# Kernel optimization log

Hardware: AMD Instinct MI355X
Metric: run time of the kernel (lower is better)

## Reference

```python
import jax, jax.numpy as jnp
import numpy as np

B, D_MODEL, D_MEM, H, N_MEM = 128, 1024, 64, 16, 4096


def setup_inputs() -> dict:
    key = jax.random.key(0)
    ks = jax.random.split(key, 6)
    scale = 1.0 / np.sqrt(D_MODEL)
    return {
        "query": jax.random.normal(ks[0], (B, D_MODEL), jnp.float32),
        "addresses": jax.random.normal(ks[1], (N_MEM, D_MEM), jnp.float32),
        "memories": jax.random.normal(ks[2], (B, N_MEM, D_MEM), jnp.float32),
        "Wq": jax.random.normal(ks[3], (D_MODEL, D_MODEL), jnp.float32) * scale,
        "bq": jnp.zeros((D_MODEL,), jnp.float32),
        "Wm": jax.random.normal(ks[4], (D_MODEL, D_MODEL), jnp.float32) * scale,
        "bm": jnp.zeros((D_MODEL,), jnp.float32),
    }


def reference(query, addresses, memories, Wq, bq, Wm, bm):
    # query projection -> heads: (B, H, d_mem)
    q = (query @ Wq.T + bq).reshape(B, H, D_MEM)
    # stage 1: build linear-attention kernel over the memory-slot dim
    k = jax.nn.relu(memories + addresses)            # (B, N, d_mem)
    matrix = jnp.einsum('bnd,bne->bde', k, memories)  # (B, d_mem, d_mem)
    normalizer = jnp.sum(k, axis=-2)                  # (B, d_mem)
    # stage 2: read the kernel with activated queries
    qa = jax.nn.relu(q)                               # (B, H, d_mem)
    numerator = jnp.einsum('bhd,bde->bhe', qa, matrix)
    denominator = jnp.einsum('bhd,bd->bh', qa, normalizer)[..., None] + 1e-5
    attn = numerator / denominator                    # (B, H, d_mem)
    return attn.reshape(B, H * D_MEM) @ Wm.T + bm     # (B, d_model)
```

## Files before the change

### kernel.cpp

```cpp
#include <hip/hip_runtime.h>
#include <hip/hip_bf16.h>

#define BATCH 128
#define DMEM 64
#define NMEM 4096
#define DMODEL 1024
#define LDS_STRIDE 40

typedef __bf16 v8bf __attribute__((ext_vector_type(8)));
typedef __bf16 v2bf __attribute__((ext_vector_type(2)));
typedef float v4f __attribute__((ext_vector_type(4)));
typedef float v16f __attribute__((ext_vector_type(16)));

__device__ __forceinline__ void gemm_sk(const float* __restrict__ A,
                                        const float* __restrict__ W,
                                        const float* __restrict__ bias,
                                        float* __restrict__ C,
                                        int m0, int n0, int k0,
                                        float* smem) {
    float(*As)[36] = (float(*)[36])smem;
    float(*Ws)[36] = (float(*)[36])(smem + 32 * 36);
    const int t = threadIdx.x;
    const int lrow = t >> 3;
    const int lc4 = (t & 7) * 4;
    const int rp = t >> 4;
    const int cp = t & 15;

    float acc00 = 0.f, acc01 = 0.f, acc10 = 0.f, acc11 = 0.f;

    v4f av = *(const v4f*)&A[(size_t)(m0 + lrow) * DMODEL + k0 + lc4];
    v4f wv = *(const v4f*)&W[(size_t)(n0 + lrow) * DMODEL + k0 + lc4];

    for (int c = 0; c < 4; ++c) {
        __syncthreads();
        *(v4f*)&As[lrow][lc4] = av;
        *(v4f*)&Ws[lrow][lc4] = wv;
        __syncthreads();
        if (c + 1 < 4) {
            const int kc = k0 + (c + 1) * 32;
            av = *(const v4f*)&A[(size_t)(m0 + lrow) * DMODEL + kc + lc4];
            wv = *(const v4f*)&W[(size_t)(n0 + lrow) * DMODEL + kc + lc4];
        }
#pragma unroll
        for (int kk = 0; kk < 32; kk += 4) {
            v4f a0 = *(v4f*)&As[rp][kk];
            v4f a1 = *(v4f*)&As[rp + 16][kk];
            v4f b0 = *(v4f*)&Ws[cp][kk];
            v4f b1 = *(v4f*)&Ws[cp + 16][kk];
#pragma unroll
            for (int q = 0; q < 4; ++q) {
                acc00 = fmaf(a0[q], b0[q], acc00);
                acc01 = fmaf(a0[q], b1[q], acc01);
                acc10 = fmaf(a1[q], b0[q], acc10);
                acc11 = fmaf(a1[q], b1[q], acc11);
            }
        }
    }
    float bv0 = 0.f, bv1 = 0.f;
    if (bias) { bv0 = bias[n0 + cp]; bv1 = bias[n0 + cp + 16]; }
    atomicAdd(&C[(size_t)(m0 + rp) * 1024 + n0 + cp], acc00 + bv0);
    atomicAdd(&C[(size_t)(m0 + rp) * 1024 + n0 + cp + 16], acc01 + bv1);
    atomicAdd(&C[(size_t)(m0 + rp + 16) * 1024 + n0 + cp], acc10 + bv0);
    atomicAdd(&C[(size_t)(m0 + rp + 16) * 1024 + n0 + cp + 16], acc11 + bv1);
}

__global__ __launch_bounds__(256, 4) void k1(const float* __restrict__ mem,
                                             const float* __restrict__ addr,
                                             float* __restrict__ pmat,
                                             float* __restrict__ pnorm,
                                             const float* __restrict__ query,
                                             const float* __restrict__ Wq,
                                             float* __restrict__ qa_ws,
                                             int S) {
    __shared__ __align__(16) char smem[24576];
    const int bid = blockIdx.x;
    const int nst = BATCH * S;

    if (bid >= nst) {
        const int b2 = bid - nst;
        const int m0 = (b2 & 3) * 32;
        const int n0 = ((b2 >> 2) & 31) * 32;
        const int ks = b2 >> 7;
        gemm_sk(query, Wq, nullptr, qa_ws, m0, n0, ks * 128, (float*)smem);
        return;
    }

    float* norm_s = (float*)(smem + 20480);

    const int t = threadIdx.x;
    const int b = bid & (BATCH - 1);
    const int s = bid >> 7;
    const int slots_per = NMEM / S;
    const int chunks = slots_per >> 5;

    const int u = t & 15;
    const int v = t >> 4;
    const int d0 = u * 4;

    const int l = t & 63;
    const int wv = t >> 6;
    const int strip = wv >> 1;
    const int kh = wv & 1;
    const int lrow = l & 31;
    const int lh = l >> 5;

    const size_t mem_base = ((size_t)b * NMEM + (size_t)s * slots_per) * DMEM;
    const size_t addr_base = (size_t)s * slots_per * DMEM;
    const size_t so = (size_t)(2 * v) * DMEM + d0;

    v16f acc0, acc1;
#pragma unroll
    for (int r = 0; r < 16; ++r) { acc0[r] = 0.f; acc1[r] = 0.f; }
    float nacc[4] = {0.f, 0.f, 0.f, 0.f};

    v4f mE0 = *(const v4f*)&mem[mem_base + so];
    v4f mE1 = *(const v4f*)&mem[mem_base + so + DMEM];
    v4f aE0 = *(const v4f*)&addr[addr_base + so];
    v4f aE1 = *(const v4f*)&addr[addr_base + so + DMEM];
    v4f mO0 = *(const v4f*)&mem[mem_base + 2048 + so];
    v4f mO1 = *(const v4f*)&mem[mem_base + 2048 + so + DMEM];
    v4f aO0 = *(const v4f*)&addr[addr_base + 2048 + so];
    v4f aO1 = *(const v4f*)&addr[addr_base + 2048 + so + DMEM];

    __bf16* kb0 = (__bf16*)smem;
    __bf16* mb0 = kb0 + 64 * LDS_STRIDE;
    __bf16* kb1 = (__bf16*)(smem + 10240);
    __bf16* mb1 = kb1 + 64 * LDS_STRIDE;
    const int cb = 16 * kh + 8 * lh;

    for (int cc = 0; cc < chunks; cc += 2) {
#pragma unroll
        for (int i = 0; i < 4; ++i) {
            float kf0 = fmaxf(mE0[i] + aE0[i], 0.f);
            float kf1 = fmaxf(mE1[i] + aE1[i], 0.f);
            nacc[i] += kf0 + kf1;
            v2bf kp; kp[0] = (__bf16)kf0; kp[1] = (__bf16)kf1;
            v2bf mp; mp[0] = (__bf16)mE0[i]; mp[1] = (__bf16)mE1[i];
            *(v2bf*)&kb0[(d0 + i) * LDS_STRIDE + 2 * v] = kp;
            *(v2bf*)&mb0[(d0 + i) * LDS_STRIDE + 2 * v] = mp;
        }
        if (cc + 2 < chunks) {
            const size_t coff = (size_t)(cc + 2) * 32 * DMEM;
            mE0 = *(const v4f*)&mem[mem_base + coff + so];
            mE1 = *(const v4f*)&mem[mem_base + coff + so + DMEM];
            aE0 = *(const v4f*)&addr[addr_base + coff + so];
            aE1 = *(const v4f*)&addr[addr_base + coff + so + DMEM];
        }
        __syncthreads();
        {
            v8bf af = *(v8bf*)&kb0[(32 * strip + lrow) * LDS_STRIDE + cb];
            v8bf b0 = *(v8bf*)&mb0[lrow * LDS_STRIDE + cb];
            v8bf b1 = *(v8bf*)&mb0[(32 + lrow) * LDS_STRIDE + cb];
            acc0 = __builtin_amdgcn_mfma_f32_32x32x16_bf16(af, b0, acc0, 0, 0, 0);
            acc1 = __builtin_amdgcn_mfma_f32_32x32x16_bf16(af, b1, acc1, 0, 0, 0);
        }
#pragma unroll
        for (int i = 0; i < 4; ++i) {
            float kf0 = fmaxf(mO0[i] + aO0[i], 0.f);
            float kf1 = fmaxf(mO1[i] + aO1[i], 0.f);
            nacc[i] += kf0 + kf1;
            v2bf kp; kp[0] = (__bf16)kf0; kp[1] = (__bf16)kf1;
            v2bf mp; mp[0] = (__bf16)mO0[i]; mp[1] = (__bf16)mO1[i];
            *(v2bf*)&kb1[(d0 + i) * LDS_STRIDE + 2 * v] = kp;
            *(v2bf*)&mb1[(d0 + i) * LDS_STRIDE + 2 * v] = mp;
        }
        if (cc + 3 < chunks) {
            const size_t coff = (size_t)(cc + 3) * 32 * DMEM;
            mO0 = *(const v4f*)&mem[mem_base + coff + so];
            mO1 = *(const v4f*)&mem[mem_base + coff + so + DMEM];
            aO0 = *(const v4f*)&addr[addr_base + coff + so];
            aO1 = *(const v4f*)&addr[addr_base + coff + so + DMEM];
        }
        __syncthreads();
        {
            v8bf af = *(v8bf*)&kb1[(32 * strip + lrow) * LDS_STRIDE + cb];
            v8bf b0 = *(v8bf*)&mb1[lrow * LDS_STRIDE + cb];
            v8bf b1 = *(v8bf*)&mb1[(32 + lrow) * LDS_STRIDE + cb];
            acc0 = __builtin_amdgcn_mfma_f32_32x32x16_bf16(af, b0, acc0, 0, 0, 0);
            acc1 = __builtin_amdgcn_mfma_f32_32x32x16_bf16(af, b1, acc1, 0, 0, 0);
        }
    }

    __syncthreads();
    float* red = (float*)smem;
#pragma unroll
    for (int i = 0; i < 4; ++i) norm_s[v * 64 + d0 + i] = nacc[i];
    if (kh == 1) {
#pragma unroll
        for (int r = 0; r < 16; ++r) {
            int row = (r & 3) + 8 * (r >> 2) + 4 * lh;
            red[strip * 2048 + row * 64 + lrow] = acc0[r];
            red[strip * 2048 + row * 64 + 32 + lrow] = acc1[r];
        }
    }
    __syncthreads();
    if (kh == 0) {
        float* pm = pmat + (size_t)bid * 4096;
#pragma unroll
        for (int r = 0; r < 16; ++r) {
            int row = (r & 3) + 8 * (r >> 2) + 4 * lh;
            int d = 32 * strip + row;
            pm[d * 64 + lrow] = acc0[r] + red[strip * 2048 + row * 64 + lrow];
            pm[d * 64 + 32 + lrow] = acc1[r] + red[strip * 2048 + row * 64 + 32 + lrow];
        }
    }
    if (t < 64) {
        float ssum = 0.f;
#pragma unroll
        for (int g = 0; g < 16; ++g) ssum += norm_s[g * 64 + t];
        pnorm[(size_t)bid * 64 + t] = ssum;
    }
}

__global__ __launch_bounds__(256) void stage2(const float* __restrict__ pmat,
                                              const float* __restrict__ pnorm,
                                              const float* __restrict__ qa_raw,
                                              const float* __restrict__ bq,
                                              float* __restrict__ attn,
                                              int S) {
    __shared__ float mat_s[4096];
    __shared__ float qa_s[1024];
    __shared__ float nrm_s[64];
    const int t = threadIdx.x;
    const int b = blockIdx.x;

#pragma unroll
    for (int i = 0; i < 4; ++i) {
        const int vi = (t + 256 * i) * 4;
        v4f ssum = (v4f){0.f, 0.f, 0.f, 0.f};
        for (int s = 0; s < S; ++s) {
            v4f p = *(const v4f*)&pmat[((size_t)s * BATCH + b) * 4096 + vi];
            ssum += p;
        }
        *(v4f*)&mat_s[vi] = ssum;
    }
    if (t < 64) {
        float ssum = 0.f;
        for (int s = 0; s < S; ++s)
            ssum += pnorm[((size_t)s * BATCH + b) * 64 + t];
        nrm_s[t] = ssum;
    }
#pragma unroll
    for (int i = 0; i < 4; ++i) {
        const int idx = t + 256 * i;
        qa_s[idx] = fmaxf(qa_raw[(size_t)b * 1024 + idx] + bq[idx], 0.f);
    }
    __syncthreads();

    const int e = t & 63;
    const int hq = t >> 6;
#pragma unroll
    for (int i = 0; i < 4; ++i) {
        const int h = hq + 4 * i;
        float num = 0.f, den = 0.f;
#pragma unroll 8
        for (int d = 0; d < 64; ++d) {
            float q = qa_s[h * 64 + d];
            num = fmaf(q, mat_s[d * 64 + e], num);
            den = fmaf(q, nrm_s[d], den);
        }
        attn[(size_t)b * 1024 + h * 64 + e] = num / (den + 1e-5f);
    }
}

__global__ __launch_bounds__(256) void gemm_sk_kernel(const float* __restrict__ A,
                                                      const float* __restrict__ W,
                                                      const float* __restrict__ bias,
                                                      float* __restrict__ C) {
    __shared__ __align__(16) float smem[2 * 32 * 36];
    const int m0 = blockIdx.x * 32;
    const int n0 = blockIdx.y * 32;
    const int ks = blockIdx.z;
    gemm_sk(A, W, ks == 0 ? bias : nullptr, C, m0, n0, ks * 128, smem);
}

extern "C" void kernel_launch(void* const* d_in, const int* in_sizes, int n_in,
                              void* d_out, int out_size, void* d_ws, size_t ws_size,
                              hipStream_t stream) {
    const float* query     = (const float*)d_in[0];
    const float* addresses = (const float*)d_in[1];
    const float* memories  = (const float*)d_in[2];
    const float* Wq        = (const float*)d_in[3];
    const float* bq        = (const float*)d_in[4];
    const float* Wm        = (const float*)d_in[5];
    const float* bm        = (const float*)d_in[6];
    float* out = (float*)d_out;
    float* ws = (float*)d_ws;

    int S = 8;
    while (S > 1) {
        size_t need = ((size_t)262144 + (size_t)S * (8192 + 524288)) * sizeof(float);
        if (need <= ws_size) break;
        S >>= 1;
    }

    float* qa_ws   = ws;
    float* attn_ws = ws + 131072;
    float* pnorm   = ws + 262144;
    float* pmat    = pnorm + (size_t)S * 8192;

    hipMemsetAsync(qa_ws, 0, 131072 * sizeof(float), stream);
    hipMemsetAsync(out, 0, (size_t)out_size * sizeof(float), stream);

    k1<<<dim3(BATCH * S + 1024), 256, 0, stream>>>(memories, addresses, pmat,
                                                   pnorm, query, Wq, qa_ws, S);
    stage2<<<dim3(BATCH), 256, 0, stream>>>(pmat, pnorm, qa_ws, bq, attn_ws, S);
    gemm_sk_kernel<<<dim3(4, 32, 8), 256, 0, stream>>>(attn_ws, Wm, bm, out);
}
```

Measured before the change: 260.6 us.

## Replace atomic split-K with partial buffers, fix slot split, widen stage2 grid

Split-K GEMM partial sums now go to separate per-slice buffers instead of atomicAdd, which removes both memsets. A new combine kernel adds the output partials plus bias, and stage2 adds the query partials. The memory-slot split is fixed at 4 instead of a runtime choice of up to 8. k1 occupancy drops from 4 to 3 blocks, and k1 writes the reduced matrix transposed through padded LDS with vectorized stores. Stage2 now runs four blocks per batch, each covering a quarter of the output columns. In exchange there is an extra kernel launch and extra partial-buffer traffic, and the code now assumes a large fixed workspace size without checking it.

```diff
diff --git a/kernel.cpp b/kernel.cpp
--- a/kernel.cpp
+++ b/kernel.cpp
@@ -5,6 +5,7 @@
 #define DMEM 64
 #define NMEM 4096
 #define DMODEL 1024
+#define S1 4
 #define LDS_STRIDE 40
 
 typedef __bf16 v8bf __attribute__((ext_vector_type(8)));
@@ -14,8 +15,7 @@
 
 __device__ __forceinline__ void gemm_sk(const float* __restrict__ A,
                                         const float* __restrict__ W,
-                                        const float* __restrict__ bias,
-                                        float* __restrict__ C,
+                                        float* __restrict__ dst,
                                         int m0, int n0, int k0,
                                         float* smem) {
     float(*As)[36] = (float(*)[36])smem;
@@ -56,32 +56,30 @@
             }
         }
     }
-    float bv0 = 0.f, bv1 = 0.f;
-    if (bias) { bv0 = bias[n0 + cp]; bv1 = bias[n0 + cp + 16]; }
-    atomicAdd(&C[(size_t)(m0 + rp) * 1024 + n0 + cp], acc00 + bv0);
-    atomicAdd(&C[(size_t)(m0 + rp) * 1024 + n0 + cp + 16], acc01 + bv1);
-    atomicAdd(&C[(size_t)(m0 + rp + 16) * 1024 + n0 + cp], acc10 + bv0);
-    atomicAdd(&C[(size_t)(m0 + rp + 16) * 1024 + n0 + cp + 16], acc11 + bv1);
-}
-
-__global__ __launch_bounds__(256, 4) void k1(const float* __restrict__ mem,
+    dst[(size_t)(m0 + rp) * DMODEL + n0 + cp] = acc00;
+    dst[(size_t)(m0 + rp) * DMODEL + n0 + cp + 16] = acc01;
+    dst[(size_t)(m0 + rp + 16) * DMODEL + n0 + cp] = acc10;
+    dst[(size_t)(m0 + rp + 16) * DMODEL + n0 + cp + 16] = acc11;
+}
+
+__global__ __launch_bounds__(256, 3) void k1(const float* __restrict__ mem,
                                              const float* __restrict__ addr,
                                              float* __restrict__ pmat,
                                              float* __restrict__ pnorm,
                                              const float* __restrict__ query,
                                              const float* __restrict__ Wq,
-                                             float* __restrict__ qa_ws,
-                                             int S) {
+                                             float* __restrict__ qa_p) {
     __shared__ __align__(16) char smem[24576];
     const int bid = blockIdx.x;
-    const int nst = BATCH * S;
+    const int nst = BATCH * S1;
 
     if (bid >= nst) {
         const int b2 = bid - nst;
         const int m0 = (b2 & 3) * 32;
         const int n0 = ((b2 >> 2) & 31) * 32;
         const int ks = b2 >> 7;
-        gemm_sk(query, Wq, nullptr, qa_ws, m0, n0, ks * 128, (float*)smem);
+        gemm_sk(query, Wq, qa_p + (size_t)ks * BATCH * DMODEL,
+                m0, n0, ks * 128, (float*)smem);
         return;
     }
 
@@ -90,7 +88,7 @@
     const int t = threadIdx.x;
     const int b = bid & (BATCH - 1);
     const int s = bid >> 7;
-    const int slots_per = NMEM / S;
+    const int slots_per = NMEM / S1;
     const int chunks = slots_per >> 5;
 
     const int u = t & 15;
@@ -189,89 +187,106 @@
 #pragma unroll
         for (int r = 0; r < 16; ++r) {
             int row = (r & 3) + 8 * (r >> 2) + 4 * lh;
-            red[strip * 2048 + row * 64 + lrow] = acc0[r];
-            red[strip * 2048 + row * 64 + 32 + lrow] = acc1[r];
+            int d = 32 * strip + row;
+            red[lrow * 68 + d] = acc0[r];
+            red[(32 + lrow) * 68 + d] = acc1[r];
         }
     }
     __syncthreads();
     if (kh == 0) {
-        float* pm = pmat + (size_t)bid * 4096;
 #pragma unroll
         for (int r = 0; r < 16; ++r) {
             int row = (r & 3) + 8 * (r >> 2) + 4 * lh;
             int d = 32 * strip + row;
-            pm[d * 64 + lrow] = acc0[r] + red[strip * 2048 + row * 64 + lrow];
-            pm[d * 64 + 32 + lrow] = acc1[r] + red[strip * 2048 + row * 64 + 32 + lrow];
-        }
+            red[lrow * 68 + d] += acc0[r];
+            red[(32 + lrow) * 68 + d] += acc1[r];
+        }
+    }
+    __syncthreads();
+    {
+        float* pm = pmat + ((size_t)s * BATCH + b) * 4096;
+        const int e = t >> 2;
+        const int ds = (t & 3) * 16;
+#pragma unroll
+        for (int j = 0; j < 4; ++j)
+            *(v4f*)&pm[e * 64 + ds + 4 * j] = *(v4f*)&red[e * 68 + ds + 4 * j];
     }
     if (t < 64) {
         float ssum = 0.f;
 #pragma unroll
         for (int g = 0; g < 16; ++g) ssum += norm_s[g * 64 + t];
-        pnorm[(size_t)bid * 64 + t] = ssum;
+        pnorm[((size_t)s * BATCH + b) * 64 + t] = ssum;
     }
 }
 
 __global__ __launch_bounds__(256) void stage2(const float* __restrict__ pmat,
                                               const float* __restrict__ pnorm,
-                                              const float* __restrict__ qa_raw,
+                                              const float* __restrict__ qa_p,
                                               const float* __restrict__ bq,
-                                              float* __restrict__ attn,
-                                              int S) {
-    __shared__ float mat_s[4096];
-    __shared__ float qa_s[1024];
+                                              float* __restrict__ attn) {
+    __shared__ float mat_s[16 * 68];
+    __shared__ float qa_s[16 * 68];
     __shared__ float nrm_s[64];
     const int t = threadIdx.x;
-    const int b = blockIdx.x;
-
+    const int b = blockIdx.x >> 2;
+    const int eq = blockIdx.x & 3;
+
+    {
+        const int i4 = t * 4;
+        v4f acc = (v4f){0.f, 0.f, 0.f, 0.f};
+#pragma unroll
+        for (int s = 0; s < S1; ++s)
+            acc += *(const v4f*)&pmat[((size_t)s * BATCH + b) * 4096 + eq * 1024 + i4];
+        *(v4f*)&mat_s[(i4 >> 6) * 68 + (i4 & 63)] = acc;
+    }
 #pragma unroll
     for (int i = 0; i < 4; ++i) {
-        const int vi = (t + 256 * i) * 4;
-        v4f ssum = (v4f){0.f, 0.f, 0.f, 0.f};
-        for (int s = 0; s < S; ++s) {
-            v4f p = *(const v4f*)&pmat[((size_t)s * BATCH + b) * 4096 + vi];
-            ssum += p;
-        }
-        *(v4f*)&mat_s[vi] = ssum;
+        const int idx = t + 256 * i;
+        float ssum = 0.f;
+#pragma unroll
+        for (int ks = 0; ks < 8; ++ks)
+            ssum += qa_p[((size_t)ks * BATCH + b) * DMODEL + idx];
+        qa_s[(idx >> 6) * 68 + (idx & 63)] = fmaxf(ssum + bq[idx], 0.f);
     }
     if (t < 64) {
         float ssum = 0.f;
-        for (int s = 0; s < S; ++s)
+#pragma unroll
+        for (int s = 0; s < S1; ++s)
             ssum += pnorm[((size_t)s * BATCH + b) * 64 + t];
         nrm_s[t] = ssum;
     }
-#pragma unroll
-    for (int i = 0; i < 4; ++i) {
-        const int idx = t + 256 * i;
-        qa_s[idx] = fmaxf(qa_raw[(size_t)b * 1024 + idx] + bq[idx], 0.f);
-    }
     __syncthreads();
 
-    const int e = t & 63;
-    const int hq = t >> 6;
-#pragma unroll
-    for (int i = 0; i < 4; ++i) {
-        const int h = hq + 4 * i;
-        float num = 0.f, den = 0.f;
+    const int h = t >> 4;
+    const int e = t & 15;
+    float num = 0.f, den = 0.f;
 #pragma unroll 8
-        for (int d = 0; d < 64; ++d) {
-            float q = qa_s[h * 64 + d];
-            num = fmaf(q, mat_s[d * 64 + e], num);
-            den = fmaf(q, nrm_s[d], den);
-        }
-        attn[(size_t)b * 1024 + h * 64 + e] = num / (den + 1e-5f);
-    }
-}
-
-__global__ __launch_bounds__(256) void gemm_sk_kernel(const float* __restrict__ A,
-                                                      const float* __restrict__ W,
-                                                      const float* __restrict__ bias,
-                                                      float* __restrict__ C) {
+    for (int d = 0; d < 64; ++d) {
+        float q = qa_s[h * 68 + d];
+        num = fmaf(q, mat_s[e * 68 + d], num);
+        den = fmaf(q, nrm_s[d], den);
+    }
+    attn[(size_t)b * DMODEL + h * 64 + eq * 16 + e] = num / (den + 1e-5f);
+}
+
+__global__ __launch_bounds__(256) void gemm_out(const float* __restrict__ A,
+                                                const float* __restrict__ W,
+                                                float* __restrict__ out_p) {
     __shared__ __align__(16) float smem[2 * 32 * 36];
-    const int m0 = blockIdx.x * 32;
-    const int n0 = blockIdx.y * 32;
     const int ks = blockIdx.z;
-    gemm_sk(A, W, ks == 0 ? bias : nullptr, C, m0, n0, ks * 128, smem);
+    gemm_sk(A, W, out_p + (size_t)ks * BATCH * DMODEL,
+            blockIdx.x * 32, blockIdx.y * 32, ks * 128, smem);
+}
+
+__global__ __launch_bounds__(256) void combine(const float* __restrict__ out_p,
+                                               const float* __restrict__ bm,
+                                               float* __restrict__ out) {
+    const int i = blockIdx.x * 256 + threadIdx.x;
+    float ssum = bm[i & (DMODEL - 1)];
+#pragma unroll
+    for (int ks = 0; ks < 8; ++ks)
+        ssum += out_p[(size_t)ks * BATCH * DMODEL + i];
+    out[i] = ssum;
 }
 
 extern "C" void kernel_launch(void* const* d_in, const int* in_sizes, int n_in,
@@ -287,23 +302,15 @@
     float* out = (float*)d_out;
     float* ws = (float*)d_ws;
 
-    int S = 8;
-    while (S > 1) {
-        size_t need = ((size_t)262144 + (size_t)S * (8192 + 524288)) * sizeof(float);
-        if (need <= ws_size) break;
-        S >>= 1;
-    }
-
-    float* qa_ws   = ws;
-    float* attn_ws = ws + 131072;
-    float* pnorm   = ws + 262144;
-    float* pmat    = pnorm + (size_t)S * 8192;
-
-    hipMemsetAsync(qa_ws, 0, 131072 * sizeof(float), stream);
-    hipMemsetAsync(out, 0, (size_t)out_size * sizeof(float), stream);
-
-    k1<<<dim3(BATCH * S + 1024), 256, 0, stream>>>(memories, addresses, pmat,
-                                                   pnorm, query, Wq, qa_ws, S);
-    stage2<<<dim3(BATCH), 256, 0, stream>>>(pmat, pnorm, qa_ws, bq, attn_ws, S);
-    gemm_sk_kernel<<<dim3(4, 32, 8), 256, 0, stream>>>(attn_ws, Wm, bm, out);
-}
+    float* qa_p    = ws;
+    float* attn_ws = qa_p + 1048576;
+    float* pnorm   = attn_ws + 131072;
+    float* pmat    = pnorm + 32768;
+    float* out_p   = pmat + 2097152;
+
+    k1<<<dim3(BATCH * S1 + 1024), 256, 0, stream>>>(memories, addresses, pmat,
+                                                    pnorm, query, Wq, qa_p);
+    stage2<<<dim3(512), 256, 0, stream>>>(pmat, pnorm, qa_p, bq, attn_ws);
+    gemm_out<<<dim3(4, 32, 8), 256, 0, stream>>>(attn_ws, Wm, out_p);
+    combine<<<dim3(512), 256, 0, stream>>>(out_p, bm, out);
+}
```

Result: faster. 226.8 us (-13.0%).
